# Kernel tuning notes

Hardware: AMD Instinct MI355X
Metric: run time of the kernel (lower is better)

## Reference

```python
import jax, jax.numpy as jnp
import numpy as np

N = 50000      # nodes
F = 128        # in_features
OUT = 128      # out_features
E = 600000     # edges per adjacency (avg degree 12)
J = 2
BN_EPS = 1e-5


def setup_inputs() -> dict:
    key = jax.random.key(0)
    ks = jax.random.split(key, 10)
    x = jax.random.normal(ks[0], (N, F), dtype=jnp.float32)
    rows0 = jax.random.randint(ks[1], (E,), 0, N, dtype=jnp.int32)
    cols0 = jax.random.randint(ks[2], (E,), 0, N, dtype=jnp.int32)
    vals0 = jax.random.uniform(ks[3], (E,), dtype=jnp.float32)
    rows1 = jax.random.randint(ks[4], (E,), 0, N, dtype=jnp.int32)
    cols1 = jax.random.randint(ks[5], (E,), 0, N, dtype=jnp.int32)
    vals1 = jax.random.uniform(ks[6], (E,), dtype=jnp.float32)
    # Linear(J*F, OUT) params, torch default init U(-1/sqrt(fan_in), 1/sqrt(fan_in))
    lim = 1.0 / np.sqrt(J * F)
    W_fc = jax.random.uniform(ks[7], (OUT, J * F), dtype=jnp.float32, minval=-lim, maxval=lim)
    b_fc = jax.random.uniform(ks[8], (OUT,), dtype=jnp.float32, minval=-lim, maxval=lim)
    gamma = jnp.ones((OUT,), dtype=jnp.float32)
    beta = jnp.zeros((OUT,), dtype=jnp.float32)
    return {"x": x, "rows0": rows0, "cols0": cols0, "vals0": vals0,
            "rows1": rows1, "cols1": cols1, "vals1": vals1,
            "W_fc": W_fc, "b_fc": b_fc, "gamma": gamma, "beta": beta}


def _spmm(rows, cols, vals, x):
    # sparse [N,N] @ dense [N,F]: gather source features, weight, scatter-add to rows
    msgs = vals[:, None] * x[cols]                      # [E, F]
    return jax.ops.segment_sum(msgs, rows, num_segments=x.shape[0])  # [N, F]


def reference(x, rows0, cols0, vals0, rows1, cols1, vals1, W_fc, b_fc, gamma, beta):
    h = jnp.concatenate([_spmm(rows0, cols0, vals0, x),
                         _spmm(rows1, cols1, vals1, x)], axis=1)  # [N, J*F]
    y = h @ W_fc.T + b_fc                                         # [N, OUT]
    # BatchNorm1d (training mode: batch stats, biased variance)
    mean = jnp.mean(y, axis=0)
    var = jnp.mean((y - mean) ** 2, axis=0)
    return (y - mean) * jax.lax.rsqrt(var + BN_EPS) * gamma + beta
```

## Files before the change

kernel.cpp:

```cpp
#include <hip/hip_runtime.h>

#define N_NODES 50000
#define F_IN 128
#define OUT_F 128
#define JF 256
#define EDGES 600000
#define BN_EPS 1e-5f
#define MAXDEG 48
#define NPART 8
#define PART_ROWS 6250
#define CHUNK_E 2048
#define NCHUNK 586

#define SCAT_B (NPART * NCHUNK)
#define CONVX_B 6250
#define CONVW_B 32
#define BUILD_B (SCAT_B + CONVX_B + CONVW_B)
#define FUSE_B 3125
#define NCOPY 16

typedef __attribute__((ext_vector_type(8))) short short8;
typedef __attribute__((ext_vector_type(4))) float floatx4;
typedef __attribute__((ext_vector_type(4))) unsigned short ushortx4;

static __device__ __forceinline__ unsigned short f2bf(float f) {
    unsigned int x = __float_as_uint(f);
    unsigned int r = (x + 0x7fffu + ((x >> 16) & 1u)) >> 16;
    return (unsigned short)r;
}
static __device__ __forceinline__ float bflo(unsigned int p) { return __uint_as_float(p << 16); }
static __device__ __forceinline__ float bfhi(unsigned int p) { return __uint_as_float(p & 0xffff0000u); }

__global__ __launch_bounds__(256) void build_kernel(
    const int* __restrict__ rows0, const int* __restrict__ cols0, const float* __restrict__ vals0,
    const int* __restrict__ rows1, const int* __restrict__ cols1, const float* __restrict__ vals1,
    int* __restrict__ cnt0, int* __restrict__ cnt1,
    unsigned int* __restrict__ pe0, unsigned int* __restrict__ pe1,
    const floatx4* __restrict__ x4, ushortx4* __restrict__ xb4,
    const floatx4* __restrict__ W4, ushortx4* __restrict__ Wb4)
{
    int bid = blockIdx.x;
    int tid = threadIdx.x;
    if (bid < SCAT_B) {
        unsigned part = (unsigned)(bid & (NPART - 1));
        int c0 = (bid >> 3) * CHUNK_E;

        bool pure0 = (c0 + CHUNK_E <= EDGES);
        bool pure1 = (c0 >= EDGES) && (c0 + CHUNK_E <= 2 * EDGES);
        if (pure0 || pure1) {
            const int*   rows = pure1 ? rows1 : rows0;
            const int*   cols = pure1 ? cols1 : cols0;
            const float* vals = pure1 ? vals1 : vals0;
            int*          cnt = pure1 ? cnt1 : cnt0;
            unsigned int*  pe = pure1 ? pe1 : pe0;
            int eb = pure1 ? c0 - EDGES : c0;
            #pragma unroll
            for (int g = 0; g < 2; ++g) {
                int e = eb + g * 1024 + tid * 4;
                int4 rv = *(const int4*)(rows + e);
                int rr[4] = {rv.x, rv.y, rv.z, rv.w};
                #pragma unroll
                for (int j = 0; j < 4; ++j) {
                    int r = rr[j];
                    if ((unsigned)r / (unsigned)PART_ROWS == part) {
                        int ee = e + j;
                        int c = cols[ee];
                        float v = vals[ee];
                        int p = atomicAdd(&cnt[r], 1);
                        if (p < MAXDEG)
                            pe[(size_t)r * MAXDEG + p] = ((unsigned int)c << 16) | f2bf(v);
                    }
                }
            }
        } else {
            for (int i = 0; i < CHUNK_E / 256; ++i) {
                int e = c0 + i * 256 + tid;
                if (e < 2 * EDGES) {
                    bool s1 = e >= EDGES;
                    int ee = s1 ? e - EDGES : e;
                    int r = s1 ? rows1[ee] : rows0[ee];
                    if ((unsigned)r / (unsigned)PART_ROWS == part) {
                        int c = s1 ? cols1[ee] : cols0[ee];
                        float v = s1 ? vals1[ee] : vals0[ee];
                        int* cnt = s1 ? cnt1 : cnt0;
                        unsigned int* pe = s1 ? pe1 : pe0;
                        int p = atomicAdd(&cnt[r], 1);
                        if (p < MAXDEG)
                            pe[(size_t)r * MAXDEG + p] = ((unsigned int)c << 16) | f2bf(v);
                    }
                }
            }
        }
    } else if (bid < SCAT_B + CONVX_B) {
        int i = (bid - SCAT_B) * 256 + tid;
        floatx4 v = __builtin_nontemporal_load(&x4[i]);
        ushortx4 o;
        o.x = f2bf(v.x); o.y = f2bf(v.y); o.z = f2bf(v.z); o.w = f2bf(v.w);
        __builtin_nontemporal_store(o, &xb4[i]);
    } else {
        int i = (bid - SCAT_B - CONVX_B) * 256 + tid;
        floatx4 v = W4[i];
        ushortx4 o;
        o.x = f2bf(v.x); o.y = f2bf(v.y); o.z = f2bf(v.z); o.w = f2bf(v.w);
        Wb4[i] = o;
    }
}

static __device__ __forceinline__ void rec2(
    unsigned int q, bool on, int lane,
    const unsigned int* __restrict__ xb32, float& A0, float& A1)
{
    unsigned int idx = on ? (q >> 16) : 0u;
    float vv = on ? __uint_as_float(q << 16) : 0.0f;
    unsigned int xv = xb32[idx * 64 + lane];
    A0 += vv * bflo(xv);
    A1 += vv * bfhi(xv);
}

__global__ __launch_bounds__(256, 4) void gather_gemm(
    const unsigned int* __restrict__ xb32,
    const int* __restrict__ cnt0, const unsigned int* __restrict__ pe0,
    const int* __restrict__ cnt1, const unsigned int* __restrict__ pe1,
    const ushort* __restrict__ Wb, const float* __restrict__ bias,
    float* __restrict__ y, float* __restrict__ stats)
{
    __shared__ unsigned int hsu[16 * 128];
    __shared__ uint4 recs[2][16][6];
    __shared__ int   lcnt[2][16];
    __shared__ float lstat[256];

    int tid = threadIdx.x;
    int lane = tid & 63;
    int w = tid >> 6;
    int wu = __builtin_amdgcn_readfirstlane(w);
    int row0 = blockIdx.x * 16;

    lstat[tid] = 0.f;

    {
        int row = tid >> 4, j = tid & 15;
        if (j < 12) {
            int side = j >= 6;
            int g = j - side * 6;
            const unsigned int* pe = side ? pe1 : pe0;
            recs[side][row][g] = *(const uint4*)(pe + (size_t)(row0 + row) * MAXDEG + g * 4);
        } else if (j == 12) {
            int d = cnt0[row0 + row]; lcnt[0][row] = d > MAXDEG ? MAXDEG : d;
        } else if (j == 13) {
            int d = cnt1[row0 + row]; lcnt[1][row] = d > MAXDEG ? MAXDEG : d;
        }
    }
    __syncthreads();

    for (int rr = 0; rr < 4; ++rr) {
        int lr = wu * 4 + rr;
        int r = row0 + lr;
        int d0 = lcnt[0][lr];
        int d1 = lcnt[1][lr];

        float aL0 = 0.f, aL1 = 0.f, aR0 = 0.f, aR1 = 0.f;

        #pragma unroll
        for (int g = 0; g < 6; ++g) {
            uint4 q = recs[0][lr][g];
            rec2(q.x, g * 4 + 0 < d0, lane, xb32, aL0, aL1);
            rec2(q.y, g * 4 + 1 < d0, lane, xb32, aL0, aL1);
            rec2(q.z, g * 4 + 2 < d0, lane, xb32, aL0, aL1);
            rec2(q.w, g * 4 + 3 < d0, lane, xb32, aL0, aL1);
        }
        #pragma unroll
        for (int g = 0; g < 6; ++g) {
            uint4 q = recs[1][lr][g];
            rec2(q.x, g * 4 + 0 < d1, lane, xb32, aR0, aR1);
            rec2(q.y, g * 4 + 1 < d1, lane, xb32, aR0, aR1);
            rec2(q.z, g * 4 + 2 < d1, lane, xb32, aR0, aR1);
            rec2(q.w, g * 4 + 3 < d1, lane, xb32, aR0, aR1);
        }
        if (d0 > 24)
            for (int p = 24; p < d0; ++p)
                rec2(pe0[(size_t)r * MAXDEG + p], true, lane, xb32, aL0, aL1);
        if (d1 > 24)
            for (int p = 24; p < d1; ++p)
                rec2(pe1[(size_t)r * MAXDEG + p], true, lane, xb32, aR0, aR1);

        unsigned int sw = (unsigned int)((lr & 7) << 4);
        unsigned int offL = ((unsigned int)(lr * 512 + lane * 4)) ^ sw;
        unsigned int offR = ((unsigned int)(lr * 512 + 256 + lane * 4)) ^ sw;
        *(unsigned int*)((char*)hsu + offL) =
            (unsigned int)f2bf(aL0) | ((unsigned int)f2bf(aL1) << 16);
        *(unsigned int*)((char*)hsu + offR) =
            (unsigned int)f2bf(aR0) | ((unsigned int)f2bf(aR1) << 16);
    }
    __syncthreads();

    floatx4 acc[2];
    acc[0] = (floatx4){0.f, 0.f, 0.f, 0.f};
    acc[1] = (floatx4){0.f, 0.f, 0.f, 0.f};

    int colb = lane & 15;
    int kg = lane >> 4;
    unsigned int asw = (unsigned int)((colb & 7) << 4);
    const char* hbase = (const char*)hsu;
    const ushort* wp = Wb + (size_t)(w * 32 + colb) * JF + kg * 8;

    #pragma unroll
    for (int k0 = 0; k0 < 8; ++k0) {
        unsigned int aoff = ((unsigned int)(colb * 512 + k0 * 64 + kg * 16)) ^ asw;
        short8 a = *(const short8*)(hbase + aoff);
        #pragma unroll
        for (int c = 0; c < 2; ++c) {
            short8 b = *(const short8*)(wp + c * 16 * JF + k0 * 32);
            acc[c] = __builtin_amdgcn_mfma_f32_16x16x32_bf16(a, b, acc[c], 0, 0, 0);
        }
    }

    int rq = kg * 4;
    #pragma unroll
    for (int c = 0; c < 2; ++c) {
        int col = w * 32 + c * 16 + colb;
        float bv = bias[col];
        float s = 0.f, s2 = 0.f;
        #pragma unroll
        for (int q = 0; q < 4; ++q) {
            float val = acc[c][q] + bv;
            y[(size_t)(row0 + rq + q) * OUT_F + col] = val;
            s += val; s2 += val * val;
        }
        atomicAdd(&lstat[col], s);
        atomicAdd(&lstat[128 + col], s2);
    }
    __syncthreads();
    float* sdst = stats + (size_t)(blockIdx.x & (NCOPY - 1)) * 256;
    atomicAdd(&sdst[tid], lstat[tid]);
}

__global__ void bn_prep(const float* __restrict__ stats,
                        const float* __restrict__ gamma,
                        const float* __restrict__ beta,
                        float* __restrict__ ss)
{
    int o = threadIdx.x;
    if (o >= OUT_F) return;
    float s = 0.f, s2 = 0.f;
    #pragma unroll
    for (int c = 0; c < NCOPY; ++c) {
        s  += stats[c * 256 + o];
        s2 += stats[c * 256 + 128 + o];
    }
    float inv_n = 1.0f / (float)N_NODES;
    float mean = s * inv_n;
    float var  = s2 * inv_n - mean * mean;
    float sc = rsqrtf(var + BN_EPS) * gamma[o];
    ss[o] = sc;
    ss[OUT_F + o] = beta[o] - mean * sc;
}

__global__ __launch_bounds__(256) void bn_apply(
    float* __restrict__ y, const float* __restrict__ ss)
{
    size_t i = (size_t)blockIdx.x * blockDim.x + threadIdx.x;
    size_t total = (size_t)N_NODES * OUT_F / 4;
    if (i >= total) return;

    int c4 = (int)(i & (OUT_F / 4 - 1));
    float4 v  = ((const float4*)y)[i];
    float4 sc = ((const float4*)ss)[c4];
    float4 sh = ((const float4*)(ss + OUT_F))[c4];
    v.x = v.x * sc.x + sh.x;
    v.y = v.y * sc.y + sh.y;
    v.z = v.z * sc.z + sh.z;
    v.w = v.w * sc.w + sh.w;
    ((float4*)y)[i] = v;
}

extern "C" void kernel_launch(void* const* d_in, const int* in_sizes, int n_in,
                              void* d_out, int out_size, void* d_ws, size_t ws_size,
                              hipStream_t stream)
{
    const float* x     = (const float*)d_in[0];
    const int*   rows0 = (const int*)  d_in[1];
    const int*   cols0 = (const int*)  d_in[2];
    const float* vals0 = (const float*)d_in[3];
    const int*   rows1 = (const int*)  d_in[4];
    const int*   cols1 = (const int*)  d_in[5];
    const float* vals1 = (const float*)d_in[6];
    const float* W     = (const float*)d_in[7];
    const float* b     = (const float*)d_in[8];
    const float* gamma = (const float*)d_in[9];
    const float* beta  = (const float*)d_in[10];

    float* y = (float*)d_out;

    ushort* xb = (ushort*)d_ws;
    ushort* Wb = xb + (size_t)N_NODES * F_IN;
    unsigned int* pe0 = (unsigned int*)(Wb + OUT_F * JF);
    unsigned int* pe1 = pe0 + (size_t)N_NODES * MAXDEG;
    int* cnt0 = (int*)(pe1 + (size_t)N_NODES * MAXDEG);
    int* cnt1 = cnt0 + N_NODES;
    float* stats = (float*)(cnt1 + N_NODES);
    float* ss    = stats + NCOPY * 256;

    hipMemsetAsync(cnt0, 0, (2 * (size_t)N_NODES + NCOPY * 256) * sizeof(int), stream);

    build_kernel<<<BUILD_B, 256, 0, stream>>>(
        rows0, cols0, vals0, rows1, cols1, vals1,
        cnt0, cnt1, pe0, pe1,
        (const floatx4*)x, (ushortx4*)xb, (const floatx4*)W, (ushortx4*)Wb);

    gather_gemm<<<FUSE_B, 256, 0, stream>>>(
        (const unsigned int*)xb, cnt0, pe0, cnt1, pe1, Wb, b, y, stats);

    bn_prep<<<1, 128, 0, stream>>>(stats, gamma, beta, ss);
    bn_apply<<<CONVX_B, 256, 0, stream>>>(y, ss);
}
```

Measured before the change: 164.2 us.

## Process 32 rows per block in fused gather-GEMM and skip empty edge groups

Doubles the rows handled per gather_gemm block from 16 to 32, halving the block count and letting each wave reuse its W fragment loads across two 16-row MFMA tiles. The edge-record loop now skips whole groups of four when the degree is below the group start, using wave-uniform degree counts, so fewer dummy gathers of row 0 are issued. Launch bounds move to 6 waves per SIMD, and tail rows past N are guarded. The trade-offs are more register and LDS use per block, fewer blocks to spread load imbalance, and new branches in the gather loop.

```diff
diff --git a/kernel.cpp b/kernel.cpp
--- a/kernel.cpp
+++ b/kernel.cpp
@@ -16,7 +16,8 @@
 #define CONVX_B 6250
 #define CONVW_B 32
 #define BUILD_B (SCAT_B + CONVX_B + CONVW_B)
-#define FUSE_B 3125
+#define ROWS_PB 32
+#define FUSE_B 1563
 #define NCOPY 16
 
 typedef __attribute__((ext_vector_type(8))) short short8;
@@ -106,7 +107,16 @@
     }
 }
 
-static __device__ __forceinline__ void rec2(
+static __device__ __forceinline__ void rec_u(
+    unsigned int q, int lane,
+    const unsigned int* __restrict__ xb32, float& A0, float& A1)
+{
+    unsigned int xv = xb32[(q >> 16) * 64 + lane];
+    float vv = __uint_as_float(q << 16);
+    A0 += vv * bflo(xv);
+    A1 += vv * bfhi(xv);
+}
+static __device__ __forceinline__ void rec_m(
     unsigned int q, bool on, int lane,
     const unsigned int* __restrict__ xb32, float& A0, float& A1)
 {
@@ -117,71 +127,87 @@
     A1 += vv * bfhi(xv);
 }
 
-__global__ __launch_bounds__(256, 4) void gather_gemm(
+__global__ __launch_bounds__(256, 6) void gather_gemm(
     const unsigned int* __restrict__ xb32,
     const int* __restrict__ cnt0, const unsigned int* __restrict__ pe0,
     const int* __restrict__ cnt1, const unsigned int* __restrict__ pe1,
     const ushort* __restrict__ Wb, const float* __restrict__ bias,
     float* __restrict__ y, float* __restrict__ stats)
 {
-    __shared__ unsigned int hsu[16 * 128];
-    __shared__ uint4 recs[2][16][6];
-    __shared__ int   lcnt[2][16];
+    __shared__ unsigned int hsu[ROWS_PB * 128];
+    __shared__ uint4 recs[2][ROWS_PB][6];
+    __shared__ int   lcnt[2][ROWS_PB];
     __shared__ float lstat[256];
 
     int tid = threadIdx.x;
     int lane = tid & 63;
     int w = tid >> 6;
     int wu = __builtin_amdgcn_readfirstlane(w);
-    int row0 = blockIdx.x * 16;
+    int row0 = blockIdx.x * ROWS_PB;
 
     lstat[tid] = 0.f;
 
     {
-        int row = tid >> 4, j = tid & 15;
-        if (j < 12) {
-            int side = j >= 6;
-            int g = j - side * 6;
-            const unsigned int* pe = side ? pe1 : pe0;
-            recs[side][row][g] = *(const uint4*)(pe + (size_t)(row0 + row) * MAXDEG + g * 4);
-        } else if (j == 12) {
-            int d = cnt0[row0 + row]; lcnt[0][row] = d > MAXDEG ? MAXDEG : d;
-        } else if (j == 13) {
-            int d = cnt1[row0 + row]; lcnt[1][row] = d > MAXDEG ? MAXDEG : d;
+        int idx = tid;
+        #pragma unroll
+        for (int pass = 0; pass < 2; ++pass) {
+            if (idx < 384) {
+                int lr = idx / 12;
+                int rem = idx - lr * 12;
+                int side = rem >= 6;
+                int g = rem - side * 6;
+                int r = row0 + lr; if (r >= N_NODES) r = N_NODES - 1;
+                const unsigned int* pe = side ? pe1 : pe0;
+                recs[side][lr][g] = *(const uint4*)(pe + (size_t)r * MAXDEG + g * 4);
+            }
+            idx += 256;
+        }
+        if (tid < 64) {
+            int side = tid >= ROWS_PB;
+            int lr = tid & (ROWS_PB - 1);
+            int r = row0 + lr;
+            int d = 0;
+            if (r < N_NODES) d = (side ? cnt1 : cnt0)[r];
+            if (d > MAXDEG) d = MAXDEG;
+            lcnt[side][lr] = d;
         }
     }
     __syncthreads();
 
-    for (int rr = 0; rr < 4; ++rr) {
-        int lr = wu * 4 + rr;
+    for (int rr = 0; rr < 8; ++rr) {
+        int lr = wu * 8 + rr;
         int r = row0 + lr;
-        int d0 = lcnt[0][lr];
-        int d1 = lcnt[1][lr];
+        int d0 = __builtin_amdgcn_readfirstlane(lcnt[0][lr]);
+        int d1 = __builtin_amdgcn_readfirstlane(lcnt[1][lr]);
 
         float aL0 = 0.f, aL1 = 0.f, aR0 = 0.f, aR1 = 0.f;
 
         #pragma unroll
         for (int g = 0; g < 6; ++g) {
-            uint4 q = recs[0][lr][g];
-            rec2(q.x, g * 4 + 0 < d0, lane, xb32, aL0, aL1);
-            rec2(q.y, g * 4 + 1 < d0, lane, xb32, aL0, aL1);
-            rec2(q.z, g * 4 + 2 < d0, lane, xb32, aL0, aL1);
-            rec2(q.w, g * 4 + 3 < d0, lane, xb32, aL0, aL1);
+            if (g * 4 < d0) {
+                uint4 q = recs[0][lr][g];
+                rec_u(q.x, lane, xb32, aL0, aL1);
+                rec_m(q.y, g * 4 + 1 < d0, lane, xb32, aL0, aL1);
+                rec_m(q.z, g * 4 + 2 < d0, lane, xb32, aL0, aL1);
+                rec_m(q.w, g * 4 + 3 < d0, lane, xb32, aL0, aL1);
+            }
         }
         #pragma unroll
         for (int g = 0; g < 6; ++g) {
-            uint4 q = recs[1][lr][g];
-            rec2(q.x, g * 4 + 0 < d1, lane, xb32, aR0, aR1);
-            rec2(q.y, g * 4 + 1 < d1, lane, xb32, aR0, aR1);
-            rec2(q.z, g * 4 + 2 < d1, lane, xb32, aR0, aR1);
-            rec2(q.w, g * 4 + 3 < d1, lane, xb32, aR0, aR1);
+            if (g * 4 < d1) {
+                uint4 q = recs[1][lr][g];
+                rec_u(q.x, lane, xb32, aR0, aR1);
+                rec_m(q.y, g * 4 + 1 < d1, lane, xb32, aR0, aR1);
+                rec_m(q.z, g * 4 + 2 < d1, lane, xb32, aR0, aR1);
+                rec_m(q.w, g * 4 + 3 < d1, lane, xb32, aR0, aR1);
+            }
         }
         if (d0 > 24)
             for (int p = 24; p < d0; ++p)
-                rec2(pe0[(size_t)r * MAXDEG + p], true, lane, xb32, aL0, aL1);
+                rec_u(pe0[(size_t)r * MAXDEG + p], lane, xb32, aL0, aL1);
         if (d1 > 24)
             for (int p = 24; p < d1; ++p)
-                rec2(pe1[(size_t)r * MAXDEG + p], true, lane, xb32, aR0, aR1);
+                rec_u(pe1[(size_t)r * MAXDEG + p], lane, xb32, aR0, aR1);
 
         unsigned int sw = (unsigned int)((lr & 7) << 4);
         unsigned int offL = ((unsigned int)(lr * 512 + lane * 4)) ^ sw;
@@ -193,41 +219,54 @@
     }
     __syncthreads();
 
-    floatx4 acc[2];
-    acc[0] = (floatx4){0.f, 0.f, 0.f, 0.f};
-    acc[1] = (floatx4){0.f, 0.f, 0.f, 0.f};
+    floatx4 acc[2][2];
+    #pragma unroll
+    for (int rt = 0; rt < 2; ++rt)
+        #pragma unroll
+        for (int c = 0; c < 2; ++c)
+            acc[rt][c] = (floatx4){0.f, 0.f, 0.f, 0.f};
 
     int colb = lane & 15;
     int kg = lane >> 4;
-    unsigned int asw = (unsigned int)((colb & 7) << 4);
     const char* hbase = (const char*)hsu;
     const ushort* wp = Wb + (size_t)(w * 32 + colb) * JF + kg * 8;
 
     #pragma unroll
     for (int k0 = 0; k0 < 8; ++k0) {
-        unsigned int aoff = ((unsigned int)(colb * 512 + k0 * 64 + kg * 16)) ^ asw;
-        short8 a = *(const short8*)(hbase + aoff);
-        #pragma unroll
-        for (int c = 0; c < 2; ++c) {
-            short8 b = *(const short8*)(wp + c * 16 * JF + k0 * 32);
-            acc[c] = __builtin_amdgcn_mfma_f32_16x16x32_bf16(a, b, acc[c], 0, 0, 0);
+        #pragma unroll
+        for (int rt = 0; rt < 2; ++rt) {
+            int arow = rt * 16 + colb;
+            unsigned int asw = (unsigned int)((arow & 7) << 4);
+            unsigned int aoff = ((unsigned int)(arow * 512 + k0 * 64 + kg * 16)) ^ asw;
+            short8 a = *(const short8*)(hbase + aoff);
+            #pragma unroll
+            for (int c = 0; c < 2; ++c) {
+                short8 b = *(const short8*)(wp + c * 16 * JF + k0 * 32);
+                acc[rt][c] = __builtin_amdgcn_mfma_f32_16x16x32_bf16(a, b, acc[rt][c], 0, 0, 0);
+            }
         }
     }
 
     int rq = kg * 4;
     #pragma unroll
-    for (int c = 0; c < 2; ++c) {
-        int col = w * 32 + c * 16 + colb;
-        float bv = bias[col];
-        float s = 0.f, s2 = 0.f;
-        #pragma unroll
-        for (int q = 0; q < 4; ++q) {
-            float val = acc[c][q] + bv;
-            y[(size_t)(row0 + rq + q) * OUT_F + col] = val;
-            s += val; s2 += val * val;
-        }
-        atomicAdd(&lstat[col], s);
-        atomicAdd(&lstat[128 + col], s2);
+    for (int rt = 0; rt < 2; ++rt) {
+        #pragma unroll
+        for (int c = 0; c < 2; ++c) {
+            int col = w * 32 + c * 16 + colb;
+            float bv = bias[col];
+            float s = 0.f, s2 = 0.f;
+            #pragma unroll
+            for (int q = 0; q < 4; ++q) {
+                int row = row0 + rt * 16 + rq + q;
+                if (row < N_NODES) {
+                    float val = acc[rt][c][q] + bv;
+                    y[(size_t)row * OUT_F + col] = val;
+                    s += val; s2 += val * val;
+                }
+            }
+            atomicAdd(&lstat[col], s);
+            atomicAdd(&lstat[128 + col], s2);
+        }
     }
     __syncthreads();
     float* sdst = stats + (size_t)(blockIdx.x & (NCOPY - 1)) * 256;
```

Result: slower. 168.3 us (+2.5%).
